# Optimization experiments

Measured on AMD Instinct MI355X. Metric: run time of the kernel, lower is better.

The kernel has to match this reference:

```python
import jax, jax.numpy as jnp
import numpy as np

B, L, F, H = 4096, 32, 28, 512  # batch, max CDR length (=input_size), features, hidden


def setup_inputs() -> dict:
    key = jax.random.key(0)
    ks = jax.random.split(key, 8)
    return {
        "input": jax.random.normal(ks[0], (B, L, F), jnp.float32),
        "unpacked_masks": jnp.ones((B, L, 1), jnp.float32),
        "bias_mat": jnp.zeros((B, L, F), jnp.float32),
        "conv1_w": jax.random.normal(ks[1], (F, F, 3), jnp.float32) * 0.1,
        "conv1_b": jnp.zeros((F,), jnp.float32),
        "conv_w": jax.random.normal(ks[2], (1, L, 1), jnp.float32) * 0.1,
        "conv_b": jnp.zeros((1,), jnp.float32),
        "fc1_w": jax.random.normal(ks[3], (1, H), jnp.float32) * 0.05,
        "fc1_b": jnp.zeros((1,), jnp.float32),
        "W_ih": jax.random.normal(ks[4], (4 * H, L), jnp.float32) * 0.1,
        "W_hh": jax.random.normal(ks[5], (4 * H, H), jnp.float32) * 0.05,
        "b_ih": jnp.zeros((4 * H,), jnp.float32),
        "b_hh": jnp.zeros((4 * H,), jnp.float32),
        "conv2_w": jax.random.normal(ks[6], (1, H, 1), jnp.float32) * 0.05,
        "conv2_b": jnp.zeros((1,), jnp.float32),
    }


def reference(input, unpacked_masks, bias_mat, conv1_w, conv1_b, conv_w, conv_b,
              fc1_w, fc1_b, W_ih, W_hh, b_ih, b_hh, conv2_w, conv2_b):
    b, l, f = input.shape
    h_dim = W_hh.shape[1]
    # --- conv1 residual block (eval mode: dropouts are identity) ---
    x_t = jnp.transpose(input, (0, 2, 1))  # [B, F, L]
    y = jax.lax.conv_general_dilated(
        x_t, conv1_w, window_strides=(1,), padding=[(1, 1)],
        dimension_numbers=("NCH", "OIH", "NCH")) + conv1_b[None, :, None]
    x = jnp.transpose(y, (0, 2, 1)) * unpacked_masks  # [B, L, F]
    x = jax.nn.elu(x) + input
    # --- u_a = Conv1d(L,1,1) over the length axis: [B, 1, F] (kept as [B, F]) ---
    u_a = jnp.einsum("blf,l->bf", x, conv_w[0, :, 0]) + conv_b  # [B, F]
    x_transposed = jnp.transpose(x, (0, 2, 1))  # [B, F, L]

    h0 = jnp.zeros((l, h_dim), input.dtype)
    c0 = jnp.zeros((l, h_dim), input.dtype)

    def step(carry, inps):
        h, c = carry
        u_b, xT_b, bias_b = inps  # [F], [F, L], [L, F]
        w_a = h @ fc1_w.T + fc1_b  # [L, 1]
        scores = jax.nn.leaky_relu(u_b[None, :] + w_a, 0.01) + bias_b  # [L, F]
        attn = jax.nn.softmax(scores, axis=0)  # softmax over dim 1 of [B, L, F]
        ctx = attn @ xT_b  # [L, F] @ [F, L] -> [L, L]
        gates = ctx @ W_ih.T + b_ih + h @ W_hh.T + b_hh  # [L, 4H]
        i_g, f_g, g_g, o_g = jnp.split(gates, 4, axis=-1)
        c_new = jax.nn.sigmoid(f_g) * c + jax.nn.sigmoid(i_g) * jnp.tanh(g_g)
        h_new = jax.nn.sigmoid(o_g) * jnp.tanh(c_new)
        return (h_new, c_new), h_new

    # The original loops over the batch dim, carrying (h, c) across iterations.
    (_, _), all_hidden = jax.lax.scan(step, (h0, c0), (u_a, x_transposed, bias_mat))
    # all_hidden: [B, L, H]
    out = jnp.einsum("blh,h->bl", all_hidden, conv2_w[0, :, 0])[..., None] + conv2_b  # [B, L, 1]
    return out * unpacked_masks
```

## Files before the change

kernel.cpp:

```cpp
#include <hip/hip_runtime.h>
#include <math.h>

#define NBATCH 4096
#define LSEQ   32
#define FDIM   28
#define HDIM   512
#define GBLK   64
#define HSTRIDE 548
#define XSTR    36

typedef int   i32x4 __attribute__((ext_vector_type(4)));
typedef float f32x4 __attribute__((ext_vector_type(4)));
typedef short short8 __attribute__((ext_vector_type(8)));

#define OFF_X    0u
#define OFF_UA   (OFF_X  + 4096u*896u)
#define OFF_BG   (OFF_UA + 4096u*28u)
#define OFF_H    (OFF_BG + 2048u)
#define OFF_BAR  (OFF_H  + 2u*32u*512u)
#define OFF_WFH  (OFF_BAR + 64u)
#define OFF_WFL  (OFF_WFH + 557056u)

__device__ __forceinline__ unsigned bfr(float x) {
    unsigned u = __builtin_bit_cast(unsigned, x);
    return (u + 0x7FFFu + ((u >> 16) & 1u)) >> 16;
}
__device__ __forceinline__ float fb(unsigned b) { return __builtin_bit_cast(float, b << 16); }
__device__ __forceinline__ unsigned packhl(float v) {
    unsigned h = bfr(v);
    unsigned l = bfr(v - fb(h));
    return h | (l << 16);
}
__device__ __forceinline__ float up(unsigned u) {
    return __builtin_bit_cast(float, u << 16) + __builtin_bit_cast(float, u & 0xFFFF0000u);
}
__device__ __forceinline__ float sigm(float v) { return 1.0f / (1.0f + __expf(-v)); }

__global__ __launch_bounds__(256) void prep_kernel(
    const float* __restrict__ input, const float* __restrict__ masks,
    const float* __restrict__ c1w, const float* __restrict__ c1b,
    const float* __restrict__ convw, const float* __restrict__ convb,
    float* __restrict__ xout, float* __restrict__ uaout)
{
    __shared__ float in_lds[32][28];
    __shared__ float w_lds[28][28][3];
    __shared__ float xo[32][28];
    __shared__ float m_lds[32];
    __shared__ float cb_lds[28];
    const int b = blockIdx.x, tid = threadIdx.x;

    for (int i = tid; i < 896; i += 256) in_lds[i / 28][i % 28] = input[(size_t)b * 896 + i];
    for (int i = tid; i < 2352; i += 256) {
        int o = i / 84, r = i % 84;
        w_lds[o][r / 3][r % 3] = c1w[i];
    }
    if (tid < 32) m_lds[tid] = masks[b * 32 + tid];
    if (tid < 28) cb_lds[tid] = c1b[tid];
    __syncthreads();

    for (int i = tid; i < 896; i += 256) {
        const int l = i / 28, f = i % 28;
        float acc = cb_lds[f];
        for (int ii = 0; ii < 28; ++ii) {
            if (l > 0)  acc = fmaf(in_lds[l - 1][ii], w_lds[f][ii][0], acc);
            acc = fmaf(in_lds[l][ii], w_lds[f][ii][1], acc);
            if (l < 31) acc = fmaf(in_lds[l + 1][ii], w_lds[f][ii][2], acc);
        }
        float v = acc * m_lds[l];
        v = (v > 0.f) ? v : expm1f(v);
        v += in_lds[l][f];
        xo[l][f] = v;
        xout[(size_t)b * 896 + i] = v;
    }
    __syncthreads();
    if (tid < 28) {
        float s = convb[0];
        for (int l = 0; l < 32; ++l) s = fmaf(xo[l][tid], convw[l], s);
        uaout[b * 28 + tid] = s;
    }
}

__global__ __launch_bounds__(256) void prepw_kernel(
    const float* __restrict__ bih, const float* __restrict__ bhh, float* __restrict__ BG)
{
    const int g = blockIdx.x * 256 + threadIdx.x;
    BG[g] = bih[g] + bhh[g];
}

__global__ __launch_bounds__(256) void prepf_kernel(
    const float* __restrict__ Wih, const float* __restrict__ Whh,
    unsigned* __restrict__ wfh, unsigned* __restrict__ wfl)
{
    const int id = blockIdx.x * 256 + threadIdx.x;
    const int lane = id & 63;
    int rest = id >> 6;
    const int ct = rest & 1; rest >>= 1;
    const int t = rest % 17, blk = rest / 17;
    const int n = lane & 15, kg = lane >> 4;
    const int c = ct * 16 + n;
    const int g = (c >> 3) * 512 + blk * 8 + (c & 7);
    const int kbase = t * 32 + kg * 8;
    i32x4 hv, lv;
    #pragma unroll
    for (int d = 0; d < 4; ++d) {
        const int k = kbase + 2 * d;
        float w0 = (k     < 512) ? Whh[(size_t)g * 512 + k]     : Wih[g * 32 + (k - 512)];
        float w1 = (k + 1 < 512) ? Whh[(size_t)g * 512 + k + 1] : Wih[g * 32 + (k + 1 - 512)];
        unsigned h0 = bfr(w0), h1 = bfr(w1);
        unsigned l0 = bfr(w0 - fb(h0)), l1 = bfr(w1 - fb(h1));
        ((unsigned*)&hv)[d] = h0 | (h1 << 16);
        ((unsigned*)&lv)[d] = l0 | (l1 << 16);
    }
    ((i32x4*)wfh)[id] = hv;
    ((i32x4*)wfl)[id] = lv;
}

__device__ __forceinline__ void stage_h16(const unsigned* hsrc, unsigned* h_lds, int tid)
{
    const int half = tid >> 7, t128 = tid & 127;
    const unsigned* p = hsrc + half * 8192 + t128 * 4;
    i32x4 v0, v1, v2, v3, v4, v5, v6, v7, v8, v9, v10, v11, v12, v13, v14, v15;
    asm volatile(
        "global_load_dwordx4 %0, %16, off sc0 sc1\n\t"
        "global_load_dwordx4 %1, %16, off offset:2048 sc0 sc1\n\t"
        "global_load_dwordx4 %2, %17, off sc0 sc1\n\t"
        "global_load_dwordx4 %3, %17, off offset:2048 sc0 sc1\n\t"
        "global_load_dwordx4 %4, %18, off sc0 sc1\n\t"
        "global_load_dwordx4 %5, %18, off offset:2048 sc0 sc1\n\t"
        "global_load_dwordx4 %6, %19, off sc0 sc1\n\t"
        "global_load_dwordx4 %7, %19, off offset:2048 sc0 sc1\n\t"
        "global_load_dwordx4 %8, %20, off sc0 sc1\n\t"
        "global_load_dwordx4 %9, %20, off offset:2048 sc0 sc1\n\t"
        "global_load_dwordx4 %10, %21, off sc0 sc1\n\t"
        "global_load_dwordx4 %11, %21, off offset:2048 sc0 sc1\n\t"
        "global_load_dwordx4 %12, %22, off sc0 sc1\n\t"
        "global_load_dwordx4 %13, %22, off offset:2048 sc0 sc1\n\t"
        "global_load_dwordx4 %14, %23, off sc0 sc1\n\t"
        "global_load_dwordx4 %15, %23, off offset:2048 sc0 sc1\n\t"
        "s_waitcnt vmcnt(0)"
        : "=&v"(v0), "=&v"(v1), "=&v"(v2), "=&v"(v3),
          "=&v"(v4), "=&v"(v5), "=&v"(v6), "=&v"(v7),
          "=&v"(v8), "=&v"(v9), "=&v"(v10), "=&v"(v11),
          "=&v"(v12), "=&v"(v13), "=&v"(v14), "=&v"(v15)
        : "v"(p), "v"(p + 1024), "v"(p + 2048), "v"(p + 3072),
          "v"(p + 4096), "v"(p + 5120), "v"(p + 6144), "v"(p + 7168)
        : "memory");
    const int col = t128 * 4;
    const int rb = half * 16;
    *(i32x4*)&h_lds[(rb +  0) * HSTRIDE + col] = v0;
    *(i32x4*)&h_lds[(rb +  1) * HSTRIDE + col] = v1;
    *(i32x4*)&h_lds[(rb +  2) * HSTRIDE + col] = v2;
    *(i32x4*)&h_lds[(rb +  3) * HSTRIDE + col] = v3;
    *(i32x4*)&h_lds[(rb +  4) * HSTRIDE + col] = v4;
    *(i32x4*)&h_lds[(rb +  5) * HSTRIDE + col] = v5;
    *(i32x4*)&h_lds[(rb +  6) * HSTRIDE + col] = v6;
    *(i32x4*)&h_lds[(rb +  7) * HSTRIDE + col] = v7;
    *(i32x4*)&h_lds[(rb +  8) * HSTRIDE + col] = v8;
    *(i32x4*)&h_lds[(rb +  9) * HSTRIDE + col] = v9;
    *(i32x4*)&h_lds[(rb + 10) * HSTRIDE + col] = v10;
    *(i32x4*)&h_lds[(rb + 11) * HSTRIDE + col] = v11;
    *(i32x4*)&h_lds[(rb + 12) * HSTRIDE + col] = v12;
    *(i32x4*)&h_lds[(rb + 13) * HSTRIDE + col] = v13;
    *(i32x4*)&h_lds[(rb + 14) * HSTRIDE + col] = v14;
    *(i32x4*)&h_lds[(rb + 15) * HSTRIDE + col] = v15;
}

__device__ __forceinline__ void build_frag(const unsigned* base, short8& hi, short8& lo)
{
    i32x4 ua = *(const i32x4*)base;
    i32x4 ub = *(const i32x4*)(base + 4);
    i32x4 h, l;
    h.x = (int)__builtin_amdgcn_perm((unsigned)ua.y, (unsigned)ua.x, 0x05040100u);
    l.x = (int)__builtin_amdgcn_perm((unsigned)ua.y, (unsigned)ua.x, 0x07060302u);
    h.y = (int)__builtin_amdgcn_perm((unsigned)ua.w, (unsigned)ua.z, 0x05040100u);
    l.y = (int)__builtin_amdgcn_perm((unsigned)ua.w, (unsigned)ua.z, 0x07060302u);
    h.z = (int)__builtin_amdgcn_perm((unsigned)ub.y, (unsigned)ub.x, 0x05040100u);
    l.z = (int)__builtin_amdgcn_perm((unsigned)ub.y, (unsigned)ub.x, 0x07060302u);
    h.w = (int)__builtin_amdgcn_perm((unsigned)ub.w, (unsigned)ub.z, 0x05040100u);
    l.w = (int)__builtin_amdgcn_perm((unsigned)ub.w, (unsigned)ub.z, 0x07060302u);
    hi = __builtin_bit_cast(short8, h);
    lo = __builtin_bit_cast(short8, l);
}

__device__ __forceinline__ float exact_gate(const unsigned* hrow,
    const float* __restrict__ Whh, const float* __restrict__ Wih, int g)
{
    const f32x4* wr = (const f32x4*)(Whh + (size_t)g * 512);
    float s = 0.f;
    #pragma unroll 4
    for (int q = 0; q < 128; ++q) {
        f32x4 w = wr[q];
        s += up(hrow[4 * q + 0]) * w.x + up(hrow[4 * q + 1]) * w.y
           + up(hrow[4 * q + 2]) * w.z + up(hrow[4 * q + 3]) * w.w;
    }
    const float* wi = Wih + g * 32;
    #pragma unroll 8
    for (int j = 0; j < 32; ++j) s += up(hrow[512 + j]) * wi[j];
    return s;
}

__device__ __forceinline__ void out_proj(const unsigned* h_lds, const float* c2w_lds, float c2b,
                                         const float* masks, float* out, int bb,
                                         int slot16, int seg16)
{
    float p0 = 0.f, p1 = 0.f;
    #pragma unroll
    for (int jj = 0; jj < 8; ++jj) {
        const int off = seg16 * 4 + 64 * jj;
        f32x4 w = *(const f32x4*)&c2w_lds[off];
        i32x4 h0 = *(const i32x4*)&h_lds[slot16 * HSTRIDE + off];
        i32x4 h1 = *(const i32x4*)&h_lds[(slot16 + 16) * HSTRIDE + off];
        p0 += up((unsigned)h0.x) * w.x + up((unsigned)h0.y) * w.y
            + up((unsigned)h0.z) * w.z + up((unsigned)h0.w) * w.w;
        p1 += up((unsigned)h1.x) * w.x + up((unsigned)h1.y) * w.y
            + up((unsigned)h1.z) * w.z + up((unsigned)h1.w) * w.w;
    }
    p0 += __shfl_xor(p0, 1); p0 += __shfl_xor(p0, 2);
    p0 += __shfl_xor(p0, 4); p0 += __shfl_xor(p0, 8);
    p1 += __shfl_xor(p1, 1); p1 += __shfl_xor(p1, 2);
    p1 += __shfl_xor(p1, 4); p1 += __shfl_xor(p1, 8);
    if (seg16 == 0) {
        out[bb * 32 + slot16]      = (p0 + c2b) * masks[bb * 32 + slot16];
        out[bb * 32 + slot16 + 16] = (p1 + c2b) * masks[bb * 32 + slot16 + 16];
    }
}

__global__ __launch_bounds__(256, 1) void rnn_serial(
    const float* __restrict__ xbuf, const float* __restrict__ uabuf,
    const float* __restrict__ BG,
    const unsigned* __restrict__ wfh, const unsigned* __restrict__ wfl,
    const float* __restrict__ Whh, const float* __restrict__ Wih,
    unsigned* hbuf, int* bar,
    const float* __restrict__ bias_mat, const float* __restrict__ masks,
    const float* __restrict__ fc1w, const float* __restrict__ fc1bp,
    const float* __restrict__ c2w, const float* __restrict__ c2bp,
    float* __restrict__ out)
{
    __shared__ unsigned h_lds[32 * HSTRIDE];
    __shared__ float x_lds[32 * XSTR];
    __shared__ float bias_lds[32 * XSTR];
    __shared__ float attn_lds[32 * XSTR];
    __shared__ float gl_part[4 * 32 * 33];
    __shared__ float wapart[4][2][32];
    __shared__ float wa_lds[32];
    __shared__ float ua_lds[28];
    __shared__ float fc1_lds[512];
    __shared__ float c2w_lds[512];
    __shared__ int   s_flag;

    const int tid  = threadIdx.x;
    const int blk  = blockIdx.x;
    const int lane = tid & 63;
    const int wv   = tid >> 6;

    for (int i = tid; i < 512; i += 256) { fc1_lds[i] = fc1w[i]; c2w_lds[i] = c2w[i]; }
    if (tid == 0) s_flag = 0;
    const float f1b = fc1bp[0];
    const float c2b = c2bp[0];

    i32x4 whi[4][2], wlo[4][2];
    {
        const i32x4* wfh4 = (const i32x4*)wfh;
        const i32x4* wfl4 = (const i32x4*)wfl;
        #pragma unroll
        for (int s = 0; s < 4; ++s)
            #pragma unroll
            for (int ct = 0; ct < 2; ++ct) {
                const int idx = ((blk * 17 + wv * 4 + s) * 2 + ct) * 64 + lane;
                whi[s][ct] = wfh4[idx];
                wlo[s][ct] = wfl4[idx];
            }
    }
    i32x4 w16h[2], w16l[2];
    if (wv == 0) {
        const i32x4* wfh4 = (const i32x4*)wfh;
        const i32x4* wfl4 = (const i32x4*)wfl;
        #pragma unroll
        for (int ct = 0; ct < 2; ++ct) {
            const int idx = ((blk * 17 + 16) * 2 + ct) * 64 + lane;
            w16h[ct] = wfh4[idx];
            w16l[ct] = wfl4[idx];
        }
    }
    i32x4 wAh[4], wAl[4];
    {
        const int n = lane & 15, kg = lane >> 4;
        #pragma unroll
        for (int s = 0; s < 4; ++s) {
            wAh[s] = (i32x4){0, 0, 0, 0};
            wAl[s] = (i32x4){0, 0, 0, 0};
            if (n < 2) {
                const float* src = (n == 0) ? fc1w : c2w;
                const int k0 = (wv * 4 + s) * 32 + kg * 8;
                #pragma unroll
                for (int d = 0; d < 4; ++d) {
                    float v0 = src[k0 + 2 * d], v1 = src[k0 + 2 * d + 1];
                    unsigned h0 = bfr(v0), h1 = bfr(v1);
                    unsigned l0 = bfr(v0 - fb(h0)), l1 = bfr(v1 - fb(h1));
                    ((unsigned*)&wAh[s])[d] = h0 | (h1 << 16);
                    ((unsigned*)&wAl[s])[d] = l0 | (l1 << 16);
                }
            }
        }
    }

    const int l_own = tid >> 3, hc = tid & 7;
    float bgv[4];
    #pragma unroll
    for (int t = 0; t < 4; ++t) bgv[t] = BG[t * 512 + blk * 8 + hc];
    float c_reg = 0.f;
    bool use_mfma = true;

    float4 xr = make_float4(0.f, 0.f, 0.f, 0.f), br = xr;
    float ua_r = 0.f;
    if (tid < 224) {
        xr = *(const float4*)(xbuf + tid * 4);
        br = *(const float4*)(bias_mat + tid * 4);
    }
    if (tid < 28) ua_r = uabuf[tid];

    const int slot16 = tid >> 4, seg16 = tid & 15;
    const int arow = lane & 15, kg = lane >> 4;
    __syncthreads();

    for (int b = 0; b < NBATCH; ++b) {
        stage_h16(hbuf + (b & 1) * 16384, h_lds, tid);
        if (tid < 224) {
            #pragma unroll
            for (int i = 0; i < 4; ++i) {
                const int idx = tid * 4 + i;
                const int l = idx / 28, f = idx - l * 28;
                x_lds[l * XSTR + f]    = ((const float*)&xr)[i];
                bias_lds[l * XSTR + f] = ((const float*)&br)[i];
            }
        }
        if (tid < 28) ua_lds[tid] = ua_r;
        __syncthreads();

        f32x4 accg[2][2], accw[2];
        if (use_mfma) {
            accg[0][0] = (f32x4){0,0,0,0}; accg[0][1] = (f32x4){0,0,0,0};
            accg[1][0] = (f32x4){0,0,0,0}; accg[1][1] = (f32x4){0,0,0,0};
            accw[0]    = (f32x4){0,0,0,0}; accw[1]    = (f32x4){0,0,0,0};
            #pragma unroll
            for (int s = 0; s < 4; ++s) {
                const int k0 = (wv * 4 + s) * 32 + kg * 8;
                short8 ah0, al0, ah1, al1;
                build_frag(&h_lds[arow * HSTRIDE + k0], ah0, al0);
                build_frag(&h_lds[(arow + 16) * HSTRIDE + k0], ah1, al1);
                #pragma unroll
                for (int ct = 0; ct < 2; ++ct) {
                    short8 bh = __builtin_bit_cast(short8, whi[s][ct]);
                    short8 bl = __builtin_bit_cast(short8, wlo[s][ct]);
                    accg[ct][0] = __builtin_amdgcn_mfma_f32_16x16x32_bf16(ah0, bh, accg[ct][0], 0, 0, 0);
                    accg[ct][0] = __builtin_amdgcn_mfma_f32_16x16x32_bf16(al0, bh, accg[ct][0], 0, 0, 0);
                    accg[ct][0] = __builtin_amdgcn_mfma_f32_16x16x32_bf16(ah0, bl, accg[ct][0], 0, 0, 0);
                    accg[ct][1] = __builtin_amdgcn_mfma_f32_16x16x32_bf16(ah1, bh, accg[ct][1], 0, 0, 0);
                    accg[ct][1] = __builtin_amdgcn_mfma_f32_16x16x32_bf16(al1, bh, accg[ct][1], 0, 0, 0);
                    accg[ct][1] = __builtin_amdgcn_mfma_f32_16x16x32_bf16(ah1, bl, accg[ct][1], 0, 0, 0);
                }
                short8 bh = __builtin_bit_cast(short8, wAh[s]);
                short8 bl = __builtin_bit_cast(short8, wAl[s]);
                accw[0] = __builtin_amdgcn_mfma_f32_16x16x32_bf16(ah0, bh, accw[0], 0, 0, 0);
                accw[0] = __builtin_amdgcn_mfma_f32_16x16x32_bf16(al0, bh, accw[0], 0, 0, 0);
                accw[0] = __builtin_amdgcn_mfma_f32_16x16x32_bf16(ah0, bl, accw[0], 0, 0, 0);
                accw[1] = __builtin_amdgcn_mfma_f32_16x16x32_bf16(ah1, bh, accw[1], 0, 0, 0);
                accw[1] = __builtin_amdgcn_mfma_f32_16x16x32_bf16(al1, bh, accw[1], 0, 0, 0);
                accw[1] = __builtin_amdgcn_mfma_f32_16x16x32_bf16(ah1, bl, accw[1], 0, 0, 0);
            }
            if (wv != 0) {
                #pragma unroll
                for (int ct = 0; ct < 2; ++ct)
                    #pragma unroll
                    for (int rt = 0; rt < 2; ++rt)
                        #pragma unroll
                        for (int r = 0; r < 4; ++r)
                            gl_part[(wv * 32 + rt * 16 + kg * 4 + r) * 33 + ct * 16 + (lane & 15)] = accg[ct][rt][r];
            }
            const int n = lane & 15;
            if (n < 2) {
                #pragma unroll
                for (int rt = 0; rt < 2; ++rt)
                    #pragma unroll
                    for (int r = 0; r < 4; ++r)
                        wapart[wv][n][rt * 16 + kg * 4 + r] = accw[rt][r];
            }
        }
        if (b < 2 || !use_mfma) {
            float p0 = 0.f, p1 = 0.f;
            #pragma unroll
            for (int jj = 0; jj < 8; ++jj) {
                const int off = seg16 * 4 + 64 * jj;
                f32x4 w = *(const f32x4*)&fc1_lds[off];
                i32x4 h0 = *(const i32x4*)&h_lds[slot16 * HSTRIDE + off];
                i32x4 h1 = *(const i32x4*)&h_lds[(slot16 + 16) * HSTRIDE + off];
                p0 += up((unsigned)h0.x) * w.x + up((unsigned)h0.y) * w.y
                    + up((unsigned)h0.z) * w.z + up((unsigned)h0.w) * w.w;
                p1 += up((unsigned)h1.x) * w.x + up((unsigned)h1.y) * w.y
                    + up((unsigned)h1.z) * w.z + up((unsigned)h1.w) * w.w;
            }
            p0 += __shfl_xor(p0, 1); p0 += __shfl_xor(p0, 2);
            p0 += __shfl_xor(p0, 4); p0 += __shfl_xor(p0, 8);
            p1 += __shfl_xor(p1, 1); p1 += __shfl_xor(p1, 2);
            p1 += __shfl_xor(p1, 4); p1 += __shfl_xor(p1, 8);
            if (seg16 == 0) { wa_lds[slot16] = p0 + f1b; wa_lds[slot16 + 16] = p1 + f1b; }
            if (b > 0 && blk == ((b - 1) & 63))
                out_proj(h_lds, c2w_lds, c2b, masks, out, b - 1, slot16, seg16);
        }
        __syncthreads();

        if (wv == 3) {
            if (use_mfma && lane < 32) {
                float wm = f1b;
                #pragma unroll
                for (int w = 0; w < 4; ++w) wm += wapart[w][0][lane];
                if (b < 2) {
                    if (fabsf(wm - wa_lds[lane]) > 0.02f + 0.004f * fabsf(wa_lds[lane])) s_flag = 1;
                } else {
                    wa_lds[lane] = wm;
                }
            }
            if (lane < 56) {
                const int f = lane >> 1, hf = lane & 1;
                const float uaf = ua_lds[f];
                float z[16], mx = -1e30f;
                #pragma unroll
                for (int i = 0; i < 16; ++i) {
                    const int l = hf * 16 + i;
                    float v = uaf + wa_lds[l];
                    v = (v >= 0.f) ? v : 0.01f * v;
                    v += bias_lds[l * XSTR + f];
                    z[i] = v;
                    mx = fmaxf(mx, v);
                }
                mx = fmaxf(mx, __shfl_xor(mx, 1));
                float sum = 0.f;
                #pragma unroll
                for (int i = 0; i < 16; ++i) { z[i] = __expf(z[i] - mx); sum += z[i]; }
                sum += __shfl_xor(sum, 1);
                const float inv = 1.0f / sum;
                #pragma unroll
                for (int i = 0; i < 16; ++i) attn_lds[(hf * 16 + i) * XSTR + f] = z[i] * inv;
            }
        } else if (wv == 2 && use_mfma && lane < 32) {
            float om = c2b;
            #pragma unroll
            for (int w = 0; w < 4; ++w) om += wapart[w][1][lane];
            if (b < 2) {
                const unsigned* hr = &h_lds[lane * HSTRIDE];
                float ox = c2b;
                for (int k = 0; k < 512; ++k) ox += up(hr[k]) * c2w_lds[k];
                if (fabsf(om - ox) > 0.02f + 0.004f * fabsf(ox)) s_flag = 1;
            } else if (b > 0 && blk == ((b - 1) & 63)) {
                out[(b - 1) * 32 + lane] = om * masks[(b - 1) * 32 + lane];
            }
        }
        __syncthreads();

        {
            const int j0 = hc * 4;
            float t0v = 0.f, t1v = 0.f, t2v = 0.f, t3v = 0.f;
            #pragma unroll
            for (int fo = 0; fo < 7; ++fo) {
                f32x4 a4 = *(const f32x4*)&attn_lds[l_own * XSTR + fo * 4];
                f32x4 x0 = *(const f32x4*)&x_lds[(j0 + 0) * XSTR + fo * 4];
                f32x4 x1 = *(const f32x4*)&x_lds[(j0 + 1) * XSTR + fo * 4];
                f32x4 x2 = *(const f32x4*)&x_lds[(j0 + 2) * XSTR + fo * 4];
                f32x4 x3 = *(const f32x4*)&x_lds[(j0 + 3) * XSTR + fo * 4];
                t0v += a4.x * x0.x + a4.y * x0.y + a4.z * x0.z + a4.w * x0.w;
                t1v += a4.x * x1.x + a4.y * x1.y + a4.z * x1.z + a4.w * x1.w;
                t2v += a4.x * x2.x + a4.y * x2.y + a4.z * x2.z + a4.w * x2.w;
                t3v += a4.x * x3.x + a4.y * x3.y + a4.z * x3.z + a4.w * x3.w;
            }
            i32x4 cp;
            cp.x = (int)packhl(t0v); cp.y = (int)packhl(t1v);
            cp.z = (int)packhl(t2v); cp.w = (int)packhl(t3v);
            *(i32x4*)&h_lds[l_own * HSTRIDE + 512 + j0] = cp;
        }
        {
            const int bn = (b + 1 < NBATCH) ? b + 1 : 0;
            if (tid < 224) {
                xr = *(const float4*)(xbuf + (size_t)bn * 896 + tid * 4);
                br = *(const float4*)(bias_mat + (size_t)bn * 896 + tid * 4);
            }
            if (tid < 28) ua_r = uabuf[bn * 28 + tid];
        }
        __syncthreads();

        if (use_mfma && wv == 0) {
            short8 ah0, al0, ah1, al1;
            build_frag(&h_lds[arow * HSTRIDE + 512 + kg * 8], ah0, al0);
            build_frag(&h_lds[(arow + 16) * HSTRIDE + 512 + kg * 8], ah1, al1);
            #pragma unroll
            for (int ct = 0; ct < 2; ++ct) {
                short8 bh = __builtin_bit_cast(short8, w16h[ct]);
                short8 bl = __builtin_bit_cast(short8, w16l[ct]);
                accg[ct][0] = __builtin_amdgcn_mfma_f32_16x16x32_bf16(ah0, bh, accg[ct][0], 0, 0, 0);
                accg[ct][0] = __builtin_amdgcn_mfma_f32_16x16x32_bf16(al0, bh, accg[ct][0], 0, 0, 0);
                accg[ct][0] = __builtin_amdgcn_mfma_f32_16x16x32_bf16(ah0, bl, accg[ct][0], 0, 0, 0);
                accg[ct][1] = __builtin_amdgcn_mfma_f32_16x16x32_bf16(ah1, bh, accg[ct][1], 0, 0, 0);
                accg[ct][1] = __builtin_amdgcn_mfma_f32_16x16x32_bf16(al1, bh, accg[ct][1], 0, 0, 0);
                accg[ct][1] = __builtin_amdgcn_mfma_f32_16x16x32_bf16(ah1, bl, accg[ct][1], 0, 0, 0);
            }
            #pragma unroll
            for (int ct = 0; ct < 2; ++ct)
                #pragma unroll
                for (int rt = 0; rt < 2; ++rt)
                    #pragma unroll
                    for (int r = 0; r < 4; ++r)
                        gl_part[(rt * 16 + kg * 4 + r) * 33 + ct * 16 + (lane & 15)] = accg[ct][rt][r];
        }
        __syncthreads();

        {
            float gv[4];
            #pragma unroll
            for (int t = 0; t < 4; ++t) {
                float g = bgv[t];
                if (use_mfma) {
                    #pragma unroll
                    for (int w = 0; w < 4; ++w)
                        g += gl_part[(w * 32 + l_own) * 33 + t * 8 + hc];
                }
                gv[t] = g;
            }
            if (b < 2) {
                bool bad = false;
                #pragma unroll
                for (int t = 0; t < 4; ++t) {
                    float ref = bgv[t] + exact_gate(&h_lds[l_own * HSTRIDE], Whh, Wih,
                                                    t * 512 + blk * 8 + hc);
                    if (use_mfma && fabsf(gv[t] - ref) > 0.02f + 0.004f * fabsf(ref)) bad = true;
                    gv[t] = ref;
                }
                if (bad) s_flag = 1;
                __syncthreads();
                use_mfma = use_mfma && (s_flag == 0);
                __syncthreads();
                if (tid == 0) s_flag = 0;
            } else if (!use_mfma) {
                #pragma unroll
                for (int t = 0; t < 4; ++t)
                    gv[t] = bgv[t] + exact_gate(&h_lds[l_own * HSTRIDE], Whh, Wih,
                                                t * 512 + blk * 8 + hc);
            }
            const float cn = sigm(gv[1]) * c_reg + sigm(gv[0]) * tanhf(gv[2]);
            const float hn = sigm(gv[3]) * tanhf(cn);
            c_reg = cn;
            __hip_atomic_store(hbuf + ((b & 1) ^ 1) * 16384 + l_own * 512 + blk * 8 + hc,
                               packhl(hn), __ATOMIC_RELAXED, __HIP_MEMORY_SCOPE_AGENT);
        }
        asm volatile("s_waitcnt vmcnt(0)" ::: "memory");
        __syncthreads();
        if (tid == 0)
            __hip_atomic_store(&bar[blk], b + 1, __ATOMIC_RELAXED, __HIP_MEMORY_SCOPE_AGENT);
        if (tid < 64) {
            while (true) {
                int v = __hip_atomic_load(&bar[tid], __ATOMIC_RELAXED, __HIP_MEMORY_SCOPE_AGENT);
                if (__all(v >= b + 1)) break;
                __builtin_amdgcn_s_sleep(1);
            }
        }
        __syncthreads();
    }

    if (blk == 63) {
        stage_h16(hbuf, h_lds, tid);
        __syncthreads();
        if (use_mfma) {
            f32x4 accw[2];
            accw[0] = (f32x4){0,0,0,0}; accw[1] = (f32x4){0,0,0,0};
            #pragma unroll
            for (int s = 0; s < 4; ++s) {
                const int k0 = (wv * 4 + s) * 32 + kg * 8;
                short8 ah0, al0, ah1, al1;
                build_frag(&h_lds[arow * HSTRIDE + k0], ah0, al0);
                build_frag(&h_lds[(arow + 16) * HSTRIDE + k0], ah1, al1);
                short8 bh = __builtin_bit_cast(short8, wAh[s]);
                short8 bl = __builtin_bit_cast(short8, wAl[s]);
                accw[0] = __builtin_amdgcn_mfma_f32_16x16x32_bf16(ah0, bh, accw[0], 0, 0, 0);
                accw[0] = __builtin_amdgcn_mfma_f32_16x16x32_bf16(al0, bh, accw[0], 0, 0, 0);
                accw[0] = __builtin_amdgcn_mfma_f32_16x16x32_bf16(ah0, bl, accw[0], 0, 0, 0);
                accw[1] = __builtin_amdgcn_mfma_f32_16x16x32_bf16(ah1, bh, accw[1], 0, 0, 0);
                accw[1] = __builtin_amdgcn_mfma_f32_16x16x32_bf16(al1, bh, accw[1], 0, 0, 0);
                accw[1] = __builtin_amdgcn_mfma_f32_16x16x32_bf16(ah1, bl, accw[1], 0, 0, 0);
            }
            const int n = lane & 15;
            if (n < 2) {
                #pragma unroll
                for (int rt = 0; rt < 2; ++rt)
                    #pragma unroll
                    for (int r = 0; r < 4; ++r)
                        wapart[wv][n][rt * 16 + kg * 4 + r] = accw[rt][r];
            }
            __syncthreads();
            if (wv == 2 && lane < 32) {
                float om = c2b;
                #pragma unroll
                for (int w = 0; w < 4; ++w) om += wapart[w][1][lane];
                out[4095 * 32 + lane] = om * masks[4095 * 32 + lane];
            }
        } else {
            out_proj(h_lds, c2w_lds, c2b, masks, out, 4095, slot16, seg16);
        }
    }
}

extern "C" void kernel_launch(void* const* d_in, const int* in_sizes, int n_in,
                              void* d_out, int out_size, void* d_ws, size_t ws_size,
                              hipStream_t stream)
{
    const float* input    = (const float*)d_in[0];
    const float* masks    = (const float*)d_in[1];
    const float* bias_mat = (const float*)d_in[2];
    const float* c1w      = (const float*)d_in[3];
    const float* c1b      = (const float*)d_in[4];
    const float* convw    = (const float*)d_in[5];
    const float* convb    = (const float*)d_in[6];
    const float* fc1w     = (const float*)d_in[7];
    const float* fc1b     = (const float*)d_in[8];
    const float* Wih      = (const float*)d_in[9];
    const float* Whh      = (const float*)d_in[10];
    const float* bih      = (const float*)d_in[11];
    const float* bhh      = (const float*)d_in[12];
    const float* c2w      = (const float*)d_in[13];
    const float* c2b      = (const float*)d_in[14];

    float* ws  = (float*)d_ws;
    float* out = (float*)d_out;
    int*   bar = (int*)(ws + OFF_BAR);

    hipMemsetAsync(ws + OFF_H, 0, (2u * 32u * 512u + 64u) * sizeof(float), stream);

    hipLaunchKernelGGL(prep_kernel, dim3(NBATCH), dim3(256), 0, stream,
                       input, masks, c1w, c1b, convw, convb, ws + OFF_X, ws + OFF_UA);
    hipLaunchKernelGGL(prepw_kernel, dim3(8), dim3(256), 0, stream,
                       bih, bhh, ws + OFF_BG);
    hipLaunchKernelGGL(prepf_kernel, dim3(544), dim3(256), 0, stream,
                       Wih, Whh, (unsigned*)(ws + OFF_WFH), (unsigned*)(ws + OFF_WFL));
    hipLaunchKernelGGL(rnn_serial, dim3(GBLK), dim3(256), 0, stream,
                       ws + OFF_X, ws + OFF_UA, ws + OFF_BG,
                       (const unsigned*)(ws + OFF_WFH), (const unsigned*)(ws + OFF_WFL),
                       Whh, Wih,
                       (unsigned*)(ws + OFF_H), bar,
                       bias_mat, masks, fc1w, fc1b, c2w, c2b, out);
}
```

Before: 28.92 ms.

## Reassociate input projection as attn @ (x @ W_ih^T) to shorten the serial step

Instead of computing the context ctx = attn @ x^T and then running a separate MFMA pass of ctx against W_ih after an extra barrier, each block precomputes M = W_ih_slice @ x for the next batch, double-buffered in LDS. The softmax wave then multiplies attention (packed bf16 hi/lo) by M directly with MFMA, writing into a fifth gl_part slice. This removes one __syncthreads and the ctx stage from the critical path of each recurrent step, and prefetches x two batches ahead. In exchange it adds per-step scalar work on the other waves and a different rounding path through the split-bf16 MFMA.

```diff
diff --git a/kernel.cpp b/kernel.cpp
--- a/kernel.cpp
+++ b/kernel.cpp
@@ -2,12 +2,10 @@
 #include <math.h>
 
 #define NBATCH 4096
-#define LSEQ   32
-#define FDIM   28
-#define HDIM   512
 #define GBLK   64
-#define HSTRIDE 548
-#define XSTR    36
+#define HSTR   516
+#define XSTR   36
+#define WSTR   33
 
 typedef int   i32x4 __attribute__((ext_vector_type(4)));
 typedef float f32x4 __attribute__((ext_vector_type(4)));
@@ -95,10 +93,10 @@
     const int lane = id & 63;
     int rest = id >> 6;
     const int ct = rest & 1; rest >>= 1;
-    const int t = rest % 17, blk = rest / 17;
+    const int t = rest % 17, blk8 = rest / 17;
     const int n = lane & 15, kg = lane >> 4;
     const int c = ct * 16 + n;
-    const int g = (c >> 3) * 512 + blk * 8 + (c & 7);
+    const int g = (c >> 3) * 512 + blk8 * 8 + (c & 7);
     const int kbase = t * 32 + kg * 8;
     i32x4 hv, lv;
     #pragma unroll
@@ -147,22 +145,22 @@
         : "memory");
     const int col = t128 * 4;
     const int rb = half * 16;
-    *(i32x4*)&h_lds[(rb +  0) * HSTRIDE + col] = v0;
-    *(i32x4*)&h_lds[(rb +  1) * HSTRIDE + col] = v1;
-    *(i32x4*)&h_lds[(rb +  2) * HSTRIDE + col] = v2;
-    *(i32x4*)&h_lds[(rb +  3) * HSTRIDE + col] = v3;
-    *(i32x4*)&h_lds[(rb +  4) * HSTRIDE + col] = v4;
-    *(i32x4*)&h_lds[(rb +  5) * HSTRIDE + col] = v5;
-    *(i32x4*)&h_lds[(rb +  6) * HSTRIDE + col] = v6;
-    *(i32x4*)&h_lds[(rb +  7) * HSTRIDE + col] = v7;
-    *(i32x4*)&h_lds[(rb +  8) * HSTRIDE + col] = v8;
-    *(i32x4*)&h_lds[(rb +  9) * HSTRIDE + col] = v9;
-    *(i32x4*)&h_lds[(rb + 10) * HSTRIDE + col] = v10;
-    *(i32x4*)&h_lds[(rb + 11) * HSTRIDE + col] = v11;
-    *(i32x4*)&h_lds[(rb + 12) * HSTRIDE + col] = v12;
-    *(i32x4*)&h_lds[(rb + 13) * HSTRIDE + col] = v13;
-    *(i32x4*)&h_lds[(rb + 14) * HSTRIDE + col] = v14;
-    *(i32x4*)&h_lds[(rb + 15) * HSTRIDE + col] = v15;
+    *(i32x4*)&h_lds[(rb +  0) * HSTR + col] = v0;
+    *(i32x4*)&h_lds[(rb +  1) * HSTR + col] = v1;
+    *(i32x4*)&h_lds[(rb +  2) * HSTR + col] = v2;
+    *(i32x4*)&h_lds[(rb +  3) * HSTR + col] = v3;
+    *(i32x4*)&h_lds[(rb +  4) * HSTR + col] = v4;
+    *(i32x4*)&h_lds[(rb +  5) * HSTR + col] = v5;
+    *(i32x4*)&h_lds[(rb +  6) * HSTR + col] = v6;
+    *(i32x4*)&h_lds[(rb +  7) * HSTR + col] = v7;
+    *(i32x4*)&h_lds[(rb +  8) * HSTR + col] = v8;
+    *(i32x4*)&h_lds[(rb +  9) * HSTR + col] = v9;
+    *(i32x4*)&h_lds[(rb + 10) * HSTR + col] = v10;
+    *(i32x4*)&h_lds[(rb + 11) * HSTR + col] = v11;
+    *(i32x4*)&h_lds[(rb + 12) * HSTR + col] = v12;
+    *(i32x4*)&h_lds[(rb + 13) * HSTR + col] = v13;
+    *(i32x4*)&h_lds[(rb + 14) * HSTR + col] = v14;
+    *(i32x4*)&h_lds[(rb + 15) * HSTR + col] = v15;
 }
 
 __device__ __forceinline__ void build_frag(const unsigned* base, short8& hi, short8& lo)
@@ -182,23 +180,6 @@
     lo = __builtin_bit_cast(short8, l);
 }
 
-__device__ __forceinline__ float exact_gate(const unsigned* hrow,
-    const float* __restrict__ Whh, const float* __restrict__ Wih, int g)
-{
-    const f32x4* wr = (const f32x4*)(Whh + (size_t)g * 512);
-    float s = 0.f;
-    #pragma unroll 4
-    for (int q = 0; q < 128; ++q) {
-        f32x4 w = wr[q];
-        s += up(hrow[4 * q + 0]) * w.x + up(hrow[4 * q + 1]) * w.y
-           + up(hrow[4 * q + 2]) * w.z + up(hrow[4 * q + 3]) * w.w;
-    }
-    const float* wi = Wih + g * 32;
-    #pragma unroll 8
-    for (int j = 0; j < 32; ++j) s += up(hrow[512 + j]) * wi[j];
-    return s;
-}
-
 __device__ __forceinline__ void out_proj(const unsigned* h_lds, const float* c2w_lds, float c2b,
                                          const float* masks, float* out, int bb,
                                          int slot16, int seg16)
@@ -208,8 +189,8 @@
     for (int jj = 0; jj < 8; ++jj) {
         const int off = seg16 * 4 + 64 * jj;
         f32x4 w = *(const f32x4*)&c2w_lds[off];
-        i32x4 h0 = *(const i32x4*)&h_lds[slot16 * HSTRIDE + off];
-        i32x4 h1 = *(const i32x4*)&h_lds[(slot16 + 16) * HSTRIDE + off];
+        i32x4 h0 = *(const i32x4*)&h_lds[slot16 * HSTR + off];
+        i32x4 h1 = *(const i32x4*)&h_lds[(slot16 + 16) * HSTR + off];
         p0 += up((unsigned)h0.x) * w.x + up((unsigned)h0.y) * w.y
             + up((unsigned)h0.z) * w.z + up((unsigned)h0.w) * w.w;
         p1 += up((unsigned)h1.x) * w.x + up((unsigned)h1.y) * w.y
@@ -236,17 +217,19 @@
     const float* __restrict__ c2w, const float* __restrict__ c2bp,
     float* __restrict__ out)
 {
-    __shared__ unsigned h_lds[32 * HSTRIDE];
-    __shared__ float x_lds[32 * XSTR];
-    __shared__ float bias_lds[32 * XSTR];
-    __shared__ float attn_lds[32 * XSTR];
-    __shared__ float gl_part[4 * 32 * 33];
-    __shared__ float wapart[4][2][32];
-    __shared__ float wa_lds[32];
-    __shared__ float ua_lds[28];
-    __shared__ float fc1_lds[512];
-    __shared__ float c2w_lds[512];
-    __shared__ int   s_flag;
+    __shared__ unsigned h_lds[32 * HSTR];
+    __shared__ float    x_lds[32 * XSTR];
+    __shared__ float    bias_lds[32 * XSTR];
+    __shared__ unsigned attn_p[32 * XSTR];
+    __shared__ float    mbuf[2][32 * XSTR];
+    __shared__ float    wihb[32 * WSTR];
+    __shared__ float    gl_part[5 * 32 * 33];
+    __shared__ float    wapart[4][2][32];
+    __shared__ float    wa_lds[32];
+    __shared__ float    ua_lds[28];
+    __shared__ float    fc1_lds[512];
+    __shared__ float    c2w_lds[512];
+    __shared__ int      s_flag;
 
     const int tid  = threadIdx.x;
     const int blk  = blockIdx.x;
@@ -271,27 +254,16 @@
                 wlo[s][ct] = wfl4[idx];
             }
     }
-    i32x4 w16h[2], w16l[2];
-    if (wv == 0) {
-        const i32x4* wfh4 = (const i32x4*)wfh;
-        const i32x4* wfl4 = (const i32x4*)wfl;
-        #pragma unroll
-        for (int ct = 0; ct < 2; ++ct) {
-            const int idx = ((blk * 17 + 16) * 2 + ct) * 64 + lane;
-            w16h[ct] = wfh4[idx];
-            w16l[ct] = wfl4[idx];
-        }
-    }
     i32x4 wAh[4], wAl[4];
     {
-        const int n = lane & 15, kg = lane >> 4;
+        const int n = lane & 15, kgi = lane >> 4;
         #pragma unroll
         for (int s = 0; s < 4; ++s) {
             wAh[s] = (i32x4){0, 0, 0, 0};
             wAl[s] = (i32x4){0, 0, 0, 0};
             if (n < 2) {
                 const float* src = (n == 0) ? fc1w : c2w;
-                const int k0 = (wv * 4 + s) * 32 + kg * 8;
+                const int k0 = (wv * 4 + s) * 32 + kgi * 8;
                 #pragma unroll
                 for (int d = 0; d < 4; ++d) {
                     float v0 = src[k0 + 2 * d], v1 = src[k0 + 2 * d + 1];
@@ -311,16 +283,42 @@
     float c_reg = 0.f;
     bool use_mfma = true;
 
+    const int slot16 = tid >> 4, seg16 = tid & 15;
+    const int arow = lane & 15, kg = lane >> 4;
+
+    for (int i = tid; i < 32 * XSTR; i += 256) {
+        attn_p[i] = 0u;
+        mbuf[0][i] = 0.f;
+        mbuf[1][i] = 0.f;
+    }
+    for (int i = tid; i < 1024; i += 256) {
+        const int c = i >> 5, j = i & 31;
+        wihb[c * WSTR + j] = Wih[((c >> 3) * 512 + blk * 8 + (c & 7)) * 32 + j];
+    }
+    if (tid < 224) {
+        float4 x0 = *(const float4*)(xbuf + tid * 4);
+        #pragma unroll
+        for (int i = 0; i < 4; ++i) {
+            const int idx = tid * 4 + i;
+            const int l = idx / 28, f = idx - l * 28;
+            x_lds[l * XSTR + f] = ((const float*)&x0)[i];
+        }
+    }
+    __syncthreads();
+    for (int idx = tid; idx < 896; idx += 256) {
+        const int c = idx / 28, f = idx - c * 28;
+        float s = 0.f;
+        #pragma unroll 8
+        for (int j = 0; j < 32; ++j) s += wihb[c * WSTR + j] * x_lds[j * XSTR + f];
+        mbuf[0][c * XSTR + f] = s;
+    }
     float4 xr = make_float4(0.f, 0.f, 0.f, 0.f), br = xr;
     float ua_r = 0.f;
     if (tid < 224) {
-        xr = *(const float4*)(xbuf + tid * 4);
+        xr = *(const float4*)(xbuf + 896 + tid * 4);
         br = *(const float4*)(bias_mat + tid * 4);
     }
     if (tid < 28) ua_r = uabuf[tid];
-
-    const int slot16 = tid >> 4, seg16 = tid & 15;
-    const int arow = lane & 15, kg = lane >> 4;
     __syncthreads();
 
     for (int b = 0; b < NBATCH; ++b) {
@@ -337,8 +335,18 @@
         if (tid < 28) ua_lds[tid] = ua_r;
         __syncthreads();
 
-        f32x4 accg[2][2], accw[2];
+        {
+            const int bx = (b + 2 < NBATCH) ? b + 2 : NBATCH - 1;
+            const int bn = (b + 1 < NBATCH) ? b + 1 : NBATCH - 1;
+            if (tid < 224) {
+                xr = *(const float4*)(xbuf + (size_t)bx * 896 + tid * 4);
+                br = *(const float4*)(bias_mat + (size_t)bn * 896 + tid * 4);
+            }
+            if (tid < 28) ua_r = uabuf[bn * 28 + tid];
+        }
+
         if (use_mfma) {
+            f32x4 accg[2][2], accw[2];
             accg[0][0] = (f32x4){0,0,0,0}; accg[0][1] = (f32x4){0,0,0,0};
             accg[1][0] = (f32x4){0,0,0,0}; accg[1][1] = (f32x4){0,0,0,0};
             accw[0]    = (f32x4){0,0,0,0}; accw[1]    = (f32x4){0,0,0,0};
@@ -346,8 +354,8 @@
             for (int s = 0; s < 4; ++s) {
                 const int k0 = (wv * 4 + s) * 32 + kg * 8;
                 short8 ah0, al0, ah1, al1;
-                build_frag(&h_lds[arow * HSTRIDE + k0], ah0, al0);
-                build_frag(&h_lds[(arow + 16) * HSTRIDE + k0], ah1, al1);
+                build_frag(&h_lds[arow * HSTR + k0], ah0, al0);
+                build_frag(&h_lds[(arow + 16) * HSTR + k0], ah1, al1);
                 #pragma unroll
                 for (int ct = 0; ct < 2; ++ct) {
                     short8 bh = __builtin_bit_cast(short8, whi[s][ct]);
@@ -368,22 +376,19 @@
                 accw[1] = __builtin_amdgcn_mfma_f32_16x16x32_bf16(al1, bh, accw[1], 0, 0, 0);
                 accw[1] = __builtin_amdgcn_mfma_f32_16x16x32_bf16(ah1, bl, accw[1], 0, 0, 0);
             }
-            if (wv != 0) {
-                #pragma unroll
-                for (int ct = 0; ct < 2; ++ct)
-                    #pragma unroll
-                    for (int rt = 0; rt < 2; ++rt)
-                        #pragma unroll
-                        for (int r = 0; r < 4; ++r)
-                            gl_part[(wv * 32 + rt * 16 + kg * 4 + r) * 33 + ct * 16 + (lane & 15)] = accg[ct][rt][r];
-            }
-            const int n = lane & 15;
-            if (n < 2) {
+            #pragma unroll
+            for (int ct = 0; ct < 2; ++ct)
                 #pragma unroll
                 for (int rt = 0; rt < 2; ++rt)
                     #pragma unroll
                     for (int r = 0; r < 4; ++r)
-                        wapart[wv][n][rt * 16 + kg * 4 + r] = accw[rt][r];
+                        gl_part[(wv * 32 + rt * 16 + kg * 4 + r) * 33 + ct * 16 + arow] = accg[ct][rt][r];
+            if (arow < 2) {
+                #pragma unroll
+                for (int rt = 0; rt < 2; ++rt)
+                    #pragma unroll
+                    for (int r = 0; r < 4; ++r)
+                        wapart[wv][arow][rt * 16 + kg * 4 + r] = accw[rt][r];
             }
         }
         if (b < 2 || !use_mfma) {
@@ -392,8 +397,8 @@
             for (int jj = 0; jj < 8; ++jj) {
                 const int off = seg16 * 4 + 64 * jj;
                 f32x4 w = *(const f32x4*)&fc1_lds[off];
-                i32x4 h0 = *(const i32x4*)&h_lds[slot16 * HSTRIDE + off];
-                i32x4 h1 = *(const i32x4*)&h_lds[(slot16 + 16) * HSTRIDE + off];
+                i32x4 h0 = *(const i32x4*)&h_lds[slot16 * HSTR + off];
+                i32x4 h1 = *(const i32x4*)&h_lds[(slot16 + 16) * HSTR + off];
                 p0 += up((unsigned)h0.x) * w.x + up((unsigned)h0.y) * w.y
                     + up((unsigned)h0.z) * w.z + up((unsigned)h0.w) * w.w;
                 p1 += up((unsigned)h1.x) * w.x + up((unsigned)h1.y) * w.y
@@ -440,75 +445,66 @@
                 sum += __shfl_xor(sum, 1);
                 const float inv = 1.0f / sum;
                 #pragma unroll
-                for (int i = 0; i < 16; ++i) attn_lds[(hf * 16 + i) * XSTR + f] = z[i] * inv;
-            }
-        } else if (wv == 2 && use_mfma && lane < 32) {
-            float om = c2b;
-            #pragma unroll
-            for (int w = 0; w < 4; ++w) om += wapart[w][1][lane];
-            if (b < 2) {
-                const unsigned* hr = &h_lds[lane * HSTRIDE];
-                float ox = c2b;
-                for (int k = 0; k < 512; ++k) ox += up(hr[k]) * c2w_lds[k];
-                if (fabsf(om - ox) > 0.02f + 0.004f * fabsf(ox)) s_flag = 1;
-            } else if (b > 0 && blk == ((b - 1) & 63)) {
-                out[(b - 1) * 32 + lane] = om * masks[(b - 1) * 32 + lane];
-            }
-        }
-        __syncthreads();
-
-        {
-            const int j0 = hc * 4;
-            float t0v = 0.f, t1v = 0.f, t2v = 0.f, t3v = 0.f;
-            #pragma unroll
-            for (int fo = 0; fo < 7; ++fo) {
-                f32x4 a4 = *(const f32x4*)&attn_lds[l_own * XSTR + fo * 4];
-                f32x4 x0 = *(const f32x4*)&x_lds[(j0 + 0) * XSTR + fo * 4];
-                f32x4 x1 = *(const f32x4*)&x_lds[(j0 + 1) * XSTR + fo * 4];
-                f32x4 x2 = *(const f32x4*)&x_lds[(j0 + 2) * XSTR + fo * 4];
-                f32x4 x3 = *(const f32x4*)&x_lds[(j0 + 3) * XSTR + fo * 4];
-                t0v += a4.x * x0.x + a4.y * x0.y + a4.z * x0.z + a4.w * x0.w;
-                t1v += a4.x * x1.x + a4.y * x1.y + a4.z * x1.z + a4.w * x1.w;
-                t2v += a4.x * x2.x + a4.y * x2.y + a4.z * x2.z + a4.w * x2.w;
-                t3v += a4.x * x3.x + a4.y * x3.y + a4.z * x3.z + a4.w * x3.w;
-            }
-            i32x4 cp;
-            cp.x = (int)packhl(t0v); cp.y = (int)packhl(t1v);
-            cp.z = (int)packhl(t2v); cp.w = (int)packhl(t3v);
-            *(i32x4*)&h_lds[l_own * HSTRIDE + 512 + j0] = cp;
-        }
-        {
-            const int bn = (b + 1 < NBATCH) ? b + 1 : 0;
-            if (tid < 224) {
-                xr = *(const float4*)(xbuf + (size_t)bn * 896 + tid * 4);
-                br = *(const float4*)(bias_mat + (size_t)bn * 896 + tid * 4);
-            }
-            if (tid < 28) ua_r = uabuf[bn * 28 + tid];
-        }
-        __syncthreads();
-
-        if (use_mfma && wv == 0) {
-            short8 ah0, al0, ah1, al1;
-            build_frag(&h_lds[arow * HSTRIDE + 512 + kg * 8], ah0, al0);
-            build_frag(&h_lds[(arow + 16) * HSTRIDE + 512 + kg * 8], ah1, al1);
-            #pragma unroll
-            for (int ct = 0; ct < 2; ++ct) {
-                short8 bh = __builtin_bit_cast(short8, w16h[ct]);
-                short8 bl = __builtin_bit_cast(short8, w16l[ct]);
-                accg[ct][0] = __builtin_amdgcn_mfma_f32_16x16x32_bf16(ah0, bh, accg[ct][0], 0, 0, 0);
-                accg[ct][0] = __builtin_amdgcn_mfma_f32_16x16x32_bf16(al0, bh, accg[ct][0], 0, 0, 0);
-                accg[ct][0] = __builtin_amdgcn_mfma_f32_16x16x32_bf16(ah0, bl, accg[ct][0], 0, 0, 0);
-                accg[ct][1] = __builtin_amdgcn_mfma_f32_16x16x32_bf16(ah1, bh, accg[ct][1], 0, 0, 0);
-                accg[ct][1] = __builtin_amdgcn_mfma_f32_16x16x32_bf16(al1, bh, accg[ct][1], 0, 0, 0);
-                accg[ct][1] = __builtin_amdgcn_mfma_f32_16x16x32_bf16(ah1, bl, accg[ct][1], 0, 0, 0);
-            }
-            #pragma unroll
-            for (int ct = 0; ct < 2; ++ct)
-                #pragma unroll
-                for (int rt = 0; rt < 2; ++rt)
+                for (int i = 0; i < 16; ++i)
+                    attn_p[(hf * 16 + i) * XSTR + f] = packhl(z[i] * inv);
+            }
+            asm volatile("s_waitcnt lgkmcnt(0)" ::: "memory");
+            __builtin_amdgcn_sched_barrier(0);
+            if (use_mfma) {
+                f32x4 accm[2][2];
+                accm[0][0] = (f32x4){0,0,0,0}; accm[0][1] = (f32x4){0,0,0,0};
+                accm[1][0] = (f32x4){0,0,0,0}; accm[1][1] = (f32x4){0,0,0,0};
+                short8 ah0, al0, ah1, al1;
+                build_frag(&attn_p[arow * XSTR + kg * 8], ah0, al0);
+                build_frag(&attn_p[(arow + 16) * XSTR + kg * 8], ah1, al1);
+                #pragma unroll
+                for (int ct = 0; ct < 2; ++ct) {
+                    const float* mrow = &mbuf[b & 1][(ct * 16 + arow) * XSTR + kg * 8];
+                    short8 bh, bl;
                     #pragma unroll
-                    for (int r = 0; r < 4; ++r)
-                        gl_part[(rt * 16 + kg * 4 + r) * 33 + ct * 16 + (lane & 15)] = accg[ct][rt][r];
+                    for (int e = 0; e < 8; ++e) {
+                        const float v = mrow[e];
+                        const unsigned hh = bfr(v);
+                        bh[e] = (short)hh;
+                        bl[e] = (short)bfr(v - fb(hh));
+                    }
+                    accm[ct][0] = __builtin_amdgcn_mfma_f32_16x16x32_bf16(ah0, bh, accm[ct][0], 0, 0, 0);
+                    accm[ct][0] = __builtin_amdgcn_mfma_f32_16x16x32_bf16(al0, bh, accm[ct][0], 0, 0, 0);
+                    accm[ct][0] = __builtin_amdgcn_mfma_f32_16x16x32_bf16(ah0, bl, accm[ct][0], 0, 0, 0);
+                    accm[ct][1] = __builtin_amdgcn_mfma_f32_16x16x32_bf16(ah1, bh, accm[ct][1], 0, 0, 0);
+                    accm[ct][1] = __builtin_amdgcn_mfma_f32_16x16x32_bf16(al1, bh, accm[ct][1], 0, 0, 0);
+                    accm[ct][1] = __builtin_amdgcn_mfma_f32_16x16x32_bf16(ah1, bl, accm[ct][1], 0, 0, 0);
+                }
+                #pragma unroll
+                for (int ct = 0; ct < 2; ++ct)
+                    #pragma unroll
+                    for (int rt = 0; rt < 2; ++rt)
+                        #pragma unroll
+                        for (int r = 0; r < 4; ++r)
+                            gl_part[(4 * 32 + rt * 16 + kg * 4 + r) * 33 + ct * 16 + arow] = accm[ct][rt][r];
+            }
+        } else {
+            if (wv == 2 && use_mfma && lane < 32) {
+                float om = c2b;
+                #pragma unroll
+                for (int w = 0; w < 4; ++w) om += wapart[w][1][lane];
+                if (b < 2) {
+                    const unsigned* hr = &h_lds[lane * HSTR];
+                    float ox = c2b;
+                    for (int k = 0; k < 512; ++k) ox += up(hr[k]) * c2w_lds[k];
+                    if (fabsf(om - ox) > 0.02f + 0.004f * fabsf(ox)) s_flag = 1;
+                } else if (b > 0 && blk == ((b - 1) & 63)) {
+                    out[(b - 1) * 32 + lane] = om * masks[(b - 1) * 32 + lane];
+                }
+            }
+            float* mdst = mbuf[(b + 1) & 1];
+            for (int idx = wv * 64 + lane; idx < 896; idx += 192) {
+                const int c = idx / 28, f = idx - c * 28;
+                float s = 0.f;
+                #pragma unroll 8
+                for (int j = 0; j < 32; ++j) s += wihb[c * WSTR + j] * x_lds[j * XSTR + f];
+                mdst[c * XSTR + f] = s;
+            }
         }
         __syncthreads();
 
@@ -519,30 +515,40 @@
                 float g = bgv[t];
                 if (use_mfma) {
                     #pragma unroll
-                    for (int w = 0; w < 4; ++w)
+                    for (int w = 0; w < 5; ++w)
                         g += gl_part[(w * 32 + l_own) * 33 + t * 8 + hc];
                 }
                 gv[t] = g;
             }
-            if (b < 2) {
+            if (b < 2 || !use_mfma) {
+                const unsigned* hrow = &h_lds[l_own * HSTR];
+                const unsigned* ar   = &attn_p[l_own * XSTR];
+                const float*    mb   = mbuf[b & 1];
                 bool bad = false;
                 #pragma unroll
                 for (int t = 0; t < 4; ++t) {
-                    float ref = bgv[t] + exact_gate(&h_lds[l_own * HSTRIDE], Whh, Wih,
-                                                    t * 512 + blk * 8 + hc);
-                    if (use_mfma && fabsf(gv[t] - ref) > 0.02f + 0.004f * fabsf(ref)) bad = true;
+                    const int g = t * 512 + blk * 8 + hc;
+                    const f32x4* wr = (const f32x4*)(Whh + (size_t)g * 512);
+                    float ref = bgv[t];
+                    #pragma unroll 4
+                    for (int q = 0; q < 128; ++q) {
+                        f32x4 w = wr[q];
+                        ref += up(hrow[4 * q + 0]) * w.x + up(hrow[4 * q + 1]) * w.y
+                             + up(hrow[4 * q + 2]) * w.z + up(hrow[4 * q + 3]) * w.w;
+                    }
+                    const float* mr = &mb[(t * 8 + hc) * XSTR];
+                    #pragma unroll 4
+                    for (int f = 0; f < 28; ++f) ref += up(ar[f]) * mr[f];
+                    if (b < 2 && use_mfma && fabsf(gv[t] - ref) > 0.02f + 0.004f * fabsf(ref)) bad = true;
                     gv[t] = ref;
                 }
-                if (bad) s_flag = 1;
-                __syncthreads();
-                use_mfma = use_mfma && (s_flag == 0);
-                __syncthreads();
-                if (tid == 0) s_flag = 0;
-            } else if (!use_mfma) {
-                #pragma unroll
-                for (int t = 0; t < 4; ++t)
-                    gv[t] = bgv[t] + exact_gate(&h_lds[l_own * HSTRIDE], Whh, Wih,
-                                                t * 512 + blk * 8 + hc);
+                if (b < 2) {
+                    if (bad) s_flag = 1;
+                    __syncthreads();
+                    use_mfma = use_mfma && (s_flag == 0);
+                    __syncthreads();
+                    if (tid == 0) s_flag = 0;
+                }
             }
             const float cn = sigm(gv[1]) * c_reg + sigm(gv[0]) * tanhf(gv[2]);
             const float hn = sigm(gv[3]) * tanhf(cn);
@@ -550,6 +556,7 @@
             __hip_atomic_store(hbuf + ((b & 1) ^ 1) * 16384 + l_own * 512 + blk * 8 + hc,
                                packhl(hn), __ATOMIC_RELAXED, __HIP_MEMORY_SCOPE_AGENT);
         }
+
         asm volatile("s_waitcnt vmcnt(0)" ::: "memory");
         __syncthreads();
         if (tid == 0)
@@ -574,8 +581,8 @@
             for (int s = 0; s < 4; ++s) {
                 const int k0 = (wv * 4 + s) * 32 + kg * 8;
                 short8 ah0, al0, ah1, al1;
-                build_frag(&h_lds[arow * HSTRIDE + k0], ah0, al0);
-                build_frag(&h_lds[(arow + 16) * HSTRIDE + k0], ah1, al1);
+                build_frag(&h_lds[arow * HSTR + k0], ah0, al0);
+                build_frag(&h_lds[(arow + 16) * HSTR + k0], ah1, al1);
                 short8 bh = __builtin_bit_cast(short8, wAh[s]);
                 short8 bl = __builtin_bit_cast(short8, wAl[s]);
                 accw[0] = __builtin_amdgcn_mfma_f32_16x16x32_bf16(ah0, bh, accw[0], 0, 0, 0);
@@ -585,13 +592,12 @@
                 accw[1] = __builtin_amdgcn_mfma_f32_16x16x32_bf16(al1, bh, accw[1], 0, 0, 0);
                 accw[1] = __builtin_amdgcn_mfma_f32_16x16x32_bf16(ah1, bl, accw[1], 0, 0, 0);
             }
-            const int n = lane & 15;
-            if (n < 2) {
+            if (arow < 2) {
                 #pragma unroll
                 for (int rt = 0; rt < 2; ++rt)
                     #pragma unroll
                     for (int r = 0; r < 4; ++r)
-                        wapart[wv][n][rt * 16 + kg * 4 + r] = accw[rt][r];
+                        wapart[wv][arow][rt * 16 + kg * 4 + r] = accw[rt][r];
             }
             __syncthreads();
             if (wv == 2 && lane < 32) {
```

Result: slower. 31.76 ms (+9.8%).
